# Kernel optimization log

Measured on AMD Instinct MI355X. Metric: run time of the kernel, lower is better.

Reference implementation:

```python
import jax, jax.numpy as jnp
import numpy as np

C = 8           # feat_channel
B, N = 8, 64    # batch, max objects
H, W = 128, 128
D = (C + 2) * C + C + C * C + C + C + 1  # 169


def setup_inputs() -> dict:
    key = jax.random.key(0)
    k1, k2, k3, k4 = jax.random.split(key, 4)
    seg_feat = jax.random.normal(k1, (B, C, H, W), dtype=jnp.float32)
    conv_weight = jax.random.normal(k2, (B, D, H, W), dtype=jnp.float32)
    mask = jnp.ones((B, N), dtype=jnp.float32)
    ind = jax.random.randint(k3, (B, N), 0, H * W, dtype=jnp.int64)
    target = jax.random.uniform(k4, (B, N, H, W), dtype=jnp.float32)
    return {"seg_feat": seg_feat, "conv_weight": conv_weight, "mask": mask,
            "ind": ind, "target": target}


def reference(seg_feat, conv_weight, mask, ind, target):
    b, c, h, w = seg_feat.shape
    n = ind.shape[1]
    # _tranpose_and_gather_feat: [B,D,H,W] -> [B,HW,D] -> gather at ind -> [B,N,D]
    wflat = conv_weight.reshape(b, -1, h * w).transpose(0, 2, 1)
    weight = jnp.take_along_axis(wflat, ind[:, :, None], axis=1)  # [B,N,D]
    splits = np.cumsum([(c + 2) * c, c, c * c, c, c])
    w1, b1, w2, b2, w3, b3 = jnp.split(weight, splits, axis=-1)
    w1 = w1.reshape(b, n, c, c + 2)   # per-object conv1 1x1 weights
    w2 = w2.reshape(b, n, c, c)
    w3 = w3.reshape(b, n, 1, c)
    # object centers and relative coordinate maps
    x0 = (ind % w).astype(jnp.float32)
    y0 = (ind // w).astype(jnp.float32)
    xg = jnp.arange(w, dtype=jnp.float32)
    yg = jnp.arange(h, dtype=jnp.float32)
    y_grid, x_grid = jnp.meshgrid(yg, xg, indexing="ij")  # [H,W]
    x_rel = (x_grid[None, None] - x0[:, :, None, None]) / 128.0  # [B,N,H,W]
    y_rel = (y_grid[None, None] - y0[:, :, None, None]) / 128.0
    feat = jnp.concatenate(
        [jnp.broadcast_to(seg_feat[:, None], (b, n, c, h, w)),
         x_rel[:, :, None], y_rel[:, :, None]], axis=2)  # [B,N,C+2,H,W]
    # three grouped 1x1 convs == per-object channel contractions
    h1 = jax.nn.relu(jnp.einsum("bnoc,bnchw->bnohw", w1, feat) + b1[..., None, None])
    h2 = jax.nn.relu(jnp.einsum("bnoc,bnchw->bnohw", w2, h1) + b2[..., None, None])
    out = jax.nn.sigmoid(jnp.einsum("bnoc,bnchw->bnohw", w3, h2) + b3[..., None, None])[:, :, 0]  # [B,N,H,W]
    m = mask[:, :, None, None]
    pred = out * m
    tgt = target * m
    smooth = 1.0
    inter = jnp.sum(pred * tgt, axis=(1, 2, 3))
    denom = jnp.sum(pred * pred, axis=(1, 2, 3)) + jnp.sum(tgt * tgt, axis=(1, 2, 3))
    loss = 1.0 - (2.0 * inter + smooth) / (denom + smooth)  # per-image dice
    return jnp.mean(loss)  # sum over batch / batch_size
```

## Files before the change

### kernel.cpp

```cpp
#include <hip/hip_runtime.h>

#define Cc 8
#define Hh 128
#define Ww 128
#define Nn 64
#define Bb 8
#define Dd 169
#define HW (Hh * Ww)
#define NP 2
#define NPG 16
#define PXS 1024
#define NSTRIPE (HW / PXS)
#define NBLK (Bb * NPG * NSTRIPE)
#define FRAGW 16
#define FRAG_U32 (256 * 64 * FRAGW)
#define SLOTS (NPG * NSTRIPE)

#define INV128 (1.0f / 128.0f)

typedef __fp16 f16x2 __attribute__((ext_vector_type(2)));
typedef _Float16 h8 __attribute__((ext_vector_type(8)));
typedef float f32x4 __attribute__((ext_vector_type(4)));

static __device__ __forceinline__ uint32_t pku(float a, float b) {
    f16x2 t = __builtin_amdgcn_cvt_pkrtz(a, b);
    uint32_t u; __builtin_memcpy(&u, &t, 4); return u;
}
static __device__ __forceinline__ h8 u4h8(uint32_t a, uint32_t b, uint32_t c, uint32_t d) {
    uint32_t u[4] = {a, b, c, d}; h8 r; __builtin_memcpy(&r, u, 16); return r;
}

__global__ void pack_frags(const float* __restrict__ conv_weight,
                           const float* __restrict__ mask,
                           const int*   __restrict__ ind,
                           uint32_t*    __restrict__ frag) {
    const int npair = blockIdx.x;
    const int b     = npair >> 5;
    const int bn0   = b * Nn + 2 * (npair & 31);
    const int l  = threadIdx.x;
    const int g  = l >> 4, r = l & 15, rr = r & 7;
    const int bnr = bn0 + (r >> 3);
    const int bng = bn0 + (g >> 1);
    const float* base = conv_weight + (size_t)b * Dd * HW;
    const float* srcR = base + ind[bnr];
    const float* srcG = base + ind[bng];

    float a1[8];
    #pragma unroll
    for (int e = 0; e < 8; ++e) {
        const int k = 8 * g + e;
        float v = 0.f;
        if (k < 8)       v = srcR[(size_t)(rr * 10 + k) * HW];
        else if (k == 8) v = srcR[(size_t)(rr * 10 + 8) * HW];
        else if (k == 9) v = srcR[(size_t)(rr * 10 + 9) * HW];
        else if (k == 10) {
            const float w8 = srcR[(size_t)(rr * 10 + 8) * HW];
            const float w9 = srcR[(size_t)(rr * 10 + 9) * HW];
            const float b1 = srcR[(size_t)(80 + rr) * HW];
            const int   ib = ind[bnr];
            v = b1 - w8 * ((float)(ib & 127) * INV128)
                   - w9 * ((float)(ib >> 7) * INV128);
        }
        a1[e] = v;
    }
    float a2[4];
    #pragma unroll
    for (int e = 0; e < 4; ++e) {
        const int k2 = 4 * g + e;
        float v = 0.f;
        if (r < 8)  { if (k2 < 8)  v = srcR[(size_t)(88 + rr * 8 + k2) * HW]; }
        else        { if (k2 >= 8) v = srcR[(size_t)(88 + rr * 8 + (k2 - 8)) * HW]; }
        a2[e] = v;
    }
    const float b2bias = (g == 0) ? srcR[(size_t)(152 + rr) * HW] : 0.f;

    float w3v[4];
    #pragma unroll
    for (int j = 0; j < 4; ++j) {
        const int c = (4 * g + j) & 7;
        w3v[j] = srcG[(size_t)(160 + c) * HW];
    }
    const float b3 = srcG[(size_t)168 * HW];
    const float mm = mask[bng];

    uint32_t* dst = frag + ((size_t)npair * 64 + l) * FRAGW;
    dst[0] = pku(a1[0], a1[1]); dst[1] = pku(a1[2], a1[3]);
    dst[2] = pku(a1[4], a1[5]); dst[3] = pku(a1[6], a1[7]);
    dst[4] = pku(a2[0], a2[1]); dst[5] = pku(a2[2], a2[3]);
    dst[6] = pku(b2bias, 0.f);
    float* df = (float*)dst;
    df[7] = w3v[0]; df[8] = w3v[1]; df[9] = w3v[2]; df[10] = w3v[3];
    df[11] = b3; df[12] = mm * mm;
    dst[13] = 0u; dst[14] = 0u; dst[15] = 0u;
}

__global__ __launch_bounds__(256)
__attribute__((amdgpu_waves_per_eu(4, 8)))
void seg_dice_main(const float* __restrict__ seg_feat,
                   const float* __restrict__ target,
                   const uint32_t* __restrict__ frag,
                   float* __restrict__ red_base) {
    const int bid    = blockIdx.x;
    const int b      = bid & 7;
    const int rest   = bid >> 3;
    const int npg    = rest & 15;
    const int stripe = rest >> 4;
    const int p0     = stripe * PXS;
    const int tid  = threadIdx.x;
    const int wave = tid >> 6;
    const int l    = tid & 63;
    const int g    = l >> 4, col = l & 15;

    __shared__ uint4 lds4[PXS];

    const float* seg_b = seg_feat + (size_t)b * Cc * HW;
    #pragma unroll
    for (int q = 0; q < 4; ++q) {
        const int px = q * 256 + tid;
        float v[8];
        #pragma unroll
        for (int c = 0; c < 8; ++c) v[c] = seg_b[(size_t)c * HW + p0 + px];
        lds4[px] = uint4{pku(v[0], v[1]), pku(v[2], v[3]),
                         pku(v[4], v[5]), pku(v[6], v[7])};
    }

    const int npair0 = b * 32 + npg * NP;
    const int par = g & 1;
    h8 A1h[NP], A2h[NP];
    float w3v[NP][4];
    float flS = 0.f, b3S = 0.f;
    const float* ptrS = target;
    #pragma unroll
    for (int j = 0; j < NP; ++j) {
        const uint4* fp = (const uint4*)(frag + ((size_t)(npair0 + j) * 64 + l) * FRAGW);
        const uint4 q0 = fp[0], q1 = fp[1], q2 = fp[2];
        const uint32_t q3x = ((const uint32_t*)fp)[12];
        A1h[j] = u4h8(q0.x, q0.y, q0.z, q0.w);
        A2h[j] = u4h8(q1.x, q1.y, q1.z, 0u);
        w3v[j][0] = __uint_as_float(q1.w);
        w3v[j][1] = __uint_as_float(q2.x);
        w3v[j][2] = __uint_as_float(q2.y);
        w3v[j][3] = __uint_as_float(q2.z);
        if (j == par) {
            b3S = __uint_as_float(q2.w);
            flS = __uint_as_float(q3x);
            const int bnS = b * Nn + 2 * (npg * NP + j) + (l >> 5);
            ptrS = target + (size_t)bnS * HW + p0 + col;
        }
    }
    __syncthreads();

    const uint32_t one16 = 0x3C00u;
    const uint32_t b2one = (g == 0) ? one16 : 0u;
    const f32x4 ZF = {0.f, 0.f, 0.f, 0.f};
    float inter = 0.f, ps = 0.f, ts = 0.f;

    #pragma unroll 1
    for (int tt = wave; tt < 64; tt += 8) {
        const int pu = tt * 16;
        const int pv = pu + 64;
        const int pxgu = p0 + pu + col;
        const int pxgv = p0 + pv + col;

        const float tvu = ptrS[pu];
        const float tvv = ptrS[pv];
        const uint4 du = lds4[pu + col];
        const uint4 dv = lds4[pv + col];

        const uint32_t xvu = pku((float)(pxgu & 127) * INV128,
                                 (float)(pxgu >> 7) * INV128);
        const uint32_t xvv = pku((float)(pxgv & 127) * INV128,
                                 (float)(pxgv >> 7) * INV128);
        const h8 B1u = u4h8((g == 0) ? du.x : ((g == 1) ? xvu : 0u),
                            (g == 0) ? du.y : ((g == 1) ? one16 : 0u),
                            (g == 0) ? du.z : 0u,
                            (g == 0) ? du.w : 0u);
        const h8 B1v = u4h8((g == 0) ? dv.x : ((g == 1) ? xvv : 0u),
                            (g == 0) ? dv.y : ((g == 1) ? one16 : 0u),
                            (g == 0) ? dv.z : 0u,
                            (g == 0) ? dv.w : 0u);

        f32x4 h1au = __builtin_amdgcn_mfma_f32_16x16x32_f16(A1h[0], B1u, ZF, 0, 0, 0);
        f32x4 h1bu = __builtin_amdgcn_mfma_f32_16x16x32_f16(A1h[1], B1u, ZF, 0, 0, 0);
        f32x4 h1av = __builtin_amdgcn_mfma_f32_16x16x32_f16(A1h[0], B1v, ZF, 0, 0, 0);
        f32x4 h1bv = __builtin_amdgcn_mfma_f32_16x16x32_f16(A1h[1], B1v, ZF, 0, 0, 0);
        #pragma unroll
        for (int e = 0; e < 4; ++e) {
            h1au[e] = fmaxf(h1au[e], 0.f); h1bu[e] = fmaxf(h1bu[e], 0.f);
            h1av[e] = fmaxf(h1av[e], 0.f); h1bv[e] = fmaxf(h1bv[e], 0.f);
        }
        const h8 B2au = u4h8(pku(h1au[0], h1au[1]), pku(h1au[2], h1au[3]), b2one, 0u);
        const h8 B2bu = u4h8(pku(h1bu[0], h1bu[1]), pku(h1bu[2], h1bu[3]), b2one, 0u);
        const h8 B2av = u4h8(pku(h1av[0], h1av[1]), pku(h1av[2], h1av[3]), b2one, 0u);
        const h8 B2bv = u4h8(pku(h1bv[0], h1bv[1]), pku(h1bv[2], h1bv[3]), b2one, 0u);

        f32x4 h2au = __builtin_amdgcn_mfma_f32_16x16x32_f16(A2h[0], B2au, ZF, 0, 0, 0);
        f32x4 h2bu = __builtin_amdgcn_mfma_f32_16x16x32_f16(A2h[1], B2bu, ZF, 0, 0, 0);
        f32x4 h2av = __builtin_amdgcn_mfma_f32_16x16x32_f16(A2h[0], B2av, ZF, 0, 0, 0);
        f32x4 h2bv = __builtin_amdgcn_mfma_f32_16x16x32_f16(A2h[1], B2bv, ZF, 0, 0, 0);

        float zpau = fmaxf(h2au[0], 0.f) * w3v[0][0];
        float zpav = fmaxf(h2av[0], 0.f) * w3v[0][0];
        zpau = fmaf(fmaxf(h2au[1], 0.f), w3v[0][1], zpau);
        zpav = fmaf(fmaxf(h2av[1], 0.f), w3v[0][1], zpav);
        zpau = fmaf(fmaxf(h2au[2], 0.f), w3v[0][2], zpau);
        zpav = fmaf(fmaxf(h2av[2], 0.f), w3v[0][2], zpav);
        zpau = fmaf(fmaxf(h2au[3], 0.f), w3v[0][3], zpau);
        zpav = fmaf(fmaxf(h2av[3], 0.f), w3v[0][3], zpav);
        float zpbu = fmaxf(h2bu[0], 0.f) * w3v[1][0];
        float zpbv = fmaxf(h2bv[0], 0.f) * w3v[1][0];
        zpbu = fmaf(fmaxf(h2bu[1], 0.f), w3v[1][1], zpbu);
        zpbv = fmaf(fmaxf(h2bv[1], 0.f), w3v[1][1], zpbv);
        zpbu = fmaf(fmaxf(h2bu[2], 0.f), w3v[1][2], zpbu);
        zpbv = fmaf(fmaxf(h2bv[2], 0.f), w3v[1][2], zpbv);
        zpbu = fmaf(fmaxf(h2bu[3], 0.f), w3v[1][3], zpbu);
        zpbv = fmaf(fmaxf(h2bv[3], 0.f), w3v[1][3], zpbv);

        zpau += __shfl_xor(zpau, 16);
        zpav += __shfl_xor(zpav, 16);
        zpbu += __shfl_xor(zpbu, 16);
        zpbv += __shfl_xor(zpbv, 16);

        const float zu = (par ? zpbu : zpau) + b3S;
        const float zv = (par ? zpbv : zpav) + b3S;
        const float ou = __builtin_amdgcn_rcpf(1.f + __expf(-zu));
        const float ov = __builtin_amdgcn_rcpf(1.f + __expf(-zv));
        const float fou = flS * ou;
        const float fov = flS * ov;
        inter = fmaf(fou, tvu, inter);
        inter = fmaf(fov, tvv, inter);
        ps    = fmaf(fou, ou, ps);
        ps    = fmaf(fov, ov, ps);
        ts    = fmaf(flS, tvu * tvu, ts);
        ts    = fmaf(flS, tvv * tvv, ts);
    }

    #pragma unroll
    for (int off = 32; off > 0; off >>= 1) {
        inter += __shfl_down(inter, off);
        ps    += __shfl_down(ps,    off);
        ts    += __shfl_down(ts,    off);
    }
    __shared__ float red[3][4];
    if ((tid & 63) == 0) { red[0][wave] = inter; red[1][wave] = ps; red[2][wave] = ts; }
    __syncthreads();
    if (tid == 0) {
        red_base[(b * 3 + 0) * SLOTS + rest] = red[0][0] + red[0][1] + red[0][2] + red[0][3];
        red_base[(b * 3 + 1) * SLOTS + rest] = red[1][0] + red[1][1] + red[1][2] + red[1][3];
        red_base[(b * 3 + 2) * SLOTS + rest] = red[2][0] + red[2][1] + red[2][2] + red[2][3];
    }
}

__global__ void seg_dice_final(const float* __restrict__ red_base, float* __restrict__ out) {
    __shared__ float red[24][4];
    const int tid = threadIdx.x;
    if (tid < 96) {
        const int series = tid >> 2;
        const int part   = tid & 3;
        const float4* p = (const float4*)(red_base + series * SLOTS + part * 64);
        float s = 0.f;
        #pragma unroll
        for (int i = 0; i < 16; ++i) { const float4 v = p[i]; s += (v.x + v.y) + (v.z + v.w); }
        red[series][part] = s;
    }
    __syncthreads();
    if (tid == 0) {
        float acc = 0.f;
        #pragma unroll
        for (int b = 0; b < Bb; ++b) {
            const float inter = red[b*3+0][0] + red[b*3+0][1] + red[b*3+0][2] + red[b*3+0][3];
            const float p2    = red[b*3+1][0] + red[b*3+1][1] + red[b*3+1][2] + red[b*3+1][3];
            const float t2    = red[b*3+2][0] + red[b*3+2][1] + red[b*3+2][2] + red[b*3+2][3];
            acc += 1.0f - (2.0f * inter + 1.0f) / (p2 + t2 + 1.0f);
        }
        out[0] = acc * (1.0f / (float)Bb);
    }
}

extern "C" void kernel_launch(void* const* d_in, const int* in_sizes, int n_in,
                              void* d_out, int out_size, void* d_ws, size_t ws_size,
                              hipStream_t stream) {
    const float* seg_feat    = (const float*)d_in[0];
    const float* conv_weight = (const float*)d_in[1];
    const float* mask        = (const float*)d_in[2];
    const int*   ind         = (const int*)d_in[3];
    const float* target      = (const float*)d_in[4];
    float* out = (float*)d_out;

    uint32_t* fragtab  = (uint32_t*)d_ws;
    float*    red_base = (float*)d_ws + FRAG_U32;

    pack_frags<<<256, 64, 0, stream>>>(conv_weight, mask, ind, fragtab);
    seg_dice_main<<<NBLK, 256, 0, stream>>>(seg_feat, target, fragtab, red_base);
    seg_dice_final<<<1, 128, 0, stream>>>(red_base, out);
}
```

Measured before the change: 35.55 us.

## Fuse final dice reduction into main kernel via atomics and last-block election

```diff
diff --git a/kernel.cpp b/kernel.cpp
--- a/kernel.cpp
+++ b/kernel.cpp
@@ -14,7 +14,6 @@
 #define NBLK (Bb * NPG * NSTRIPE)
 #define FRAGW 16
 #define FRAG_U32 (256 * 64 * FRAGW)
-#define SLOTS (NPG * NSTRIPE)
 
 #define INV128 (1.0f / 128.0f)
 
@@ -34,10 +33,10 @@
                            const float* __restrict__ mask,
                            const int*   __restrict__ ind,
                            uint32_t*    __restrict__ frag) {
-    const int npair = blockIdx.x;
+    const int npair = blockIdx.x * 4 + (threadIdx.x >> 6);
     const int b     = npair >> 5;
     const int bn0   = b * Nn + 2 * (npair & 31);
-    const int l  = threadIdx.x;
+    const int l  = threadIdx.x & 63;
     const int g  = l >> 4, r = l & 15, rr = r & 7;
     const int bnr = bn0 + (r >> 3);
     const int bng = bn0 + (g >> 1);
@@ -99,7 +98,9 @@
 void seg_dice_main(const float* __restrict__ seg_feat,
                    const float* __restrict__ target,
                    const uint32_t* __restrict__ frag,
-                   float* __restrict__ red_base) {
+                   float* __restrict__ acc,
+                   unsigned* __restrict__ cnt,
+                   float* __restrict__ out) {
     const int bid    = blockIdx.x;
     const int b      = bid & 7;
     const int rest   = bid >> 3;
@@ -245,35 +246,26 @@
     if ((tid & 63) == 0) { red[0][wave] = inter; red[1][wave] = ps; red[2][wave] = ts; }
     __syncthreads();
     if (tid == 0) {
-        red_base[(b * 3 + 0) * SLOTS + rest] = red[0][0] + red[0][1] + red[0][2] + red[0][3];
-        red_base[(b * 3 + 1) * SLOTS + rest] = red[1][0] + red[1][1] + red[1][2] + red[1][3];
-        red_base[(b * 3 + 2) * SLOTS + rest] = red[2][0] + red[2][1] + red[2][2] + red[2][3];
-    }
-}
-
-__global__ void seg_dice_final(const float* __restrict__ red_base, float* __restrict__ out) {
-    __shared__ float red[24][4];
-    const int tid = threadIdx.x;
-    if (tid < 96) {
-        const int series = tid >> 2;
-        const int part   = tid & 3;
-        const float4* p = (const float4*)(red_base + series * SLOTS + part * 64);
-        float s = 0.f;
-        #pragma unroll
-        for (int i = 0; i < 16; ++i) { const float4 v = p[i]; s += (v.x + v.y) + (v.z + v.w); }
-        red[series][part] = s;
-    }
-    __syncthreads();
-    if (tid == 0) {
-        float acc = 0.f;
-        #pragma unroll
-        for (int b = 0; b < Bb; ++b) {
-            const float inter = red[b*3+0][0] + red[b*3+0][1] + red[b*3+0][2] + red[b*3+0][3];
-            const float p2    = red[b*3+1][0] + red[b*3+1][1] + red[b*3+1][2] + red[b*3+1][3];
-            const float t2    = red[b*3+2][0] + red[b*3+2][1] + red[b*3+2][2] + red[b*3+2][3];
-            acc += 1.0f - (2.0f * inter + 1.0f) / (p2 + t2 + 1.0f);
-        }
-        out[0] = acc * (1.0f / (float)Bb);
+        const float i2 = red[0][0] + red[0][1] + red[0][2] + red[0][3];
+        const float p2 = red[1][0] + red[1][1] + red[1][2] + red[1][3];
+        const float t2 = red[2][0] + red[2][1] + red[2][2] + red[2][3];
+        atomicAdd(&acc[b * 3 + 0], i2);
+        atomicAdd(&acc[b * 3 + 1], p2);
+        atomicAdd(&acc[b * 3 + 2], t2);
+        __threadfence();
+        const unsigned done = atomicAdd(cnt, 1u);
+        if (done == (unsigned)(NBLK - 1)) {
+            __threadfence();
+            float loss = 0.f;
+            #pragma unroll
+            for (int bb = 0; bb < Bb; ++bb) {
+                const float I = atomicAdd(&acc[bb * 3 + 0], 0.f);
+                const float P = atomicAdd(&acc[bb * 3 + 1], 0.f);
+                const float T = atomicAdd(&acc[bb * 3 + 2], 0.f);
+                loss += 1.f - (2.f * I + 1.f) / (P + T + 1.f);
+            }
+            out[0] = loss * (1.f / (float)Bb);
+        }
     }
 }
 
@@ -287,10 +279,12 @@
     const float* target      = (const float*)d_in[4];
     float* out = (float*)d_out;
 
-    uint32_t* fragtab  = (uint32_t*)d_ws;
-    float*    red_base = (float*)d_ws + FRAG_U32;
-
-    pack_frags<<<256, 64, 0, stream>>>(conv_weight, mask, ind, fragtab);
-    seg_dice_main<<<NBLK, 256, 0, stream>>>(seg_feat, target, fragtab, red_base);
-    seg_dice_final<<<1, 128, 0, stream>>>(red_base, out);
-}
+    uint32_t* fragtab = (uint32_t*)d_ws;
+    float*    acc     = (float*)d_ws + FRAG_U32;
+    unsigned* cnt     = (unsigned*)(acc + 24);
+
+    hipMemsetAsync(acc, 0, 25 * sizeof(float), stream);
+
+    pack_frags<<<64, 256, 0, stream>>>(conv_weight, mask, ind, fragtab);
+    seg_dice_main<<<NBLK, 256, 0, stream>>>(seg_feat, target, fragtab, acc, cnt, out);
+}
```

Result: slower. 101.3 us (+185.0%).
